# Performance work log

Measured on AMD Instinct MI355X. Metric: run time of the kernel, lower is better.

## Reference

```python
import jax, jax.numpy as jnp
import numpy as np

B, T, D = 2, 2048, 1024
NUM_HEAD = 8
HEAD_DIM = D // NUM_HEAD
CLIP = 2  # _RELATIVE_POS_CLIP


def setup_inputs() -> dict:
    key = jax.random.key(0)
    ks = jax.random.split(key, 12)
    s = 0.02
    return {
        "query": jax.random.normal(ks[0], (B, T, D), jnp.float32),
        "keys": jax.random.normal(ks[1], (B, T, D), jnp.float32),
        "values": jax.random.normal(ks[2], (B, T, D), jnp.float32),
        "Wq": jax.random.normal(ks[3], (D, D), jnp.float32) * s,
        "bq": jnp.zeros((D,), jnp.float32),
        "Wk": jax.random.normal(ks[4], (D, D), jnp.float32) * s,
        "bk": jnp.zeros((D,), jnp.float32),
        "Wv": jax.random.normal(ks[5], (D, D), jnp.float32) * s,
        "bv": jnp.zeros((D,), jnp.float32),
        "Wo": jax.random.normal(ks[6], (D, D), jnp.float32) * s,
        "bo": jnp.zeros((D,), jnp.float32),
        "relpos_table": jax.random.normal(ks[7], (2 * CLIP + 1, D), jnp.float32) * s,
    }


def reference(query, keys, values, Wq, bq, Wk, bk, Wv, bv, Wo, bo, relpos_table):
    Bq, T2, _ = query.shape
    T1 = keys.shape[1]
    # QKV projections (torch Linear: y = x @ W.T + b)
    tq = query @ Wq.T + bq                      # (B, T2, D)
    tk = keys @ Wk.T + bk                       # (B, T1, D)
    tv = values @ Wv.T + bv                     # (B, T1, D)

    # relative-position logits: relpos_embed[i,j] = table[clip(j-i)+CLIP]
    # faithful math via (B,T2,5) dots + gather instead of (T2,T1,D) broadcast
    relpos = jnp.clip(jnp.arange(T1)[None, :] - jnp.arange(T2)[:, None],
                      -CLIP, CLIP) + CLIP        # (T2, T1) int
    proj = tq @ relpos_table.T                   # (B, T2, 2*CLIP+1)
    relpos_logits = proj[:, jnp.arange(T2)[:, None], relpos]  # (B, T2, T1)

    # split heads
    q = tq.reshape(Bq, T2, NUM_HEAD, HEAD_DIM).transpose(0, 2, 1, 3)
    k = tk.reshape(Bq, T1, NUM_HEAD, HEAD_DIM).transpose(0, 2, 1, 3)
    v = tv.reshape(Bq, T1, NUM_HEAD, HEAD_DIM).transpose(0, 2, 1, 3)

    logits = jnp.einsum("bhqd,bhkd->bhqk", q, k)
    logits = (logits + relpos_logits[:, None]) / jnp.sqrt(
        jnp.asarray(HEAD_DIM, logits.dtype))    # scaling after bias, as in nmtlab
    weights = jax.nn.softmax(logits, axis=-1)   # (B, H, T2, T1)
    ctx = jnp.einsum("bhqk,bhkd->bhqd", weights, v)
    ctx = ctx.transpose(0, 2, 1, 3).reshape(Bq, T2, NUM_HEAD * HEAD_DIM)
    out = ctx @ Wo.T + bo                        # (B, T2, D)
    return out, weights
```

## Files before the change

kernel.cpp:

```cpp
#include <hip/hip_runtime.h>
#include <hip/hip_bf16.h>
#include <cmath>

#define Bsz 2
#define Tsz 2048
#define Dsz 1024
#define Hn  8
#define DH  128
#define SCALE 0.08838834764831845f

typedef __attribute__((ext_vector_type(8))) short short8;
typedef __attribute__((ext_vector_type(4))) short short4v;
typedef __attribute__((ext_vector_type(4))) float f32x4;
typedef __hip_bfloat16 bf16;

#define LDK 136

__device__ __forceinline__ float bf2f(unsigned short u) {
    return __uint_as_float(((unsigned)u) << 16);
}
__device__ __forceinline__ unsigned short f2bf(float f) {
    bf16 h = __float2bfloat16(f);
    return *(unsigned short*)&h;
}
__device__ __forceinline__ short8 pack8(float4 a, float4 b) {
    short8 o;
    o[0] = (short)f2bf(a.x); o[1] = (short)f2bf(a.y);
    o[2] = (short)f2bf(a.z); o[3] = (short)f2bf(a.w);
    o[4] = (short)f2bf(b.x); o[5] = (short)f2bf(b.y);
    o[6] = (short)f2bf(b.z); o[7] = (short)f2bf(b.w);
    return o;
}

__device__ __forceinline__ void gload16(const bf16* g, bf16* l) {
    __builtin_amdgcn_global_load_lds(
        (const __attribute__((address_space(1))) void*)g,
        (__attribute__((address_space(3))) void*)l, 16, 0, 0);
}

struct CvtJob { const float* s; bf16* d; int n; };
struct CvtArgs { CvtJob j[4]; };

__global__ __launch_bounds__(256) void cvt_k(CvtArgs a) {
    CvtJob job = a.j[blockIdx.y];
    int idx = (blockIdx.x * 256 + threadIdx.x) * 8;
    const int stride = gridDim.x * 256 * 8;
    for (; idx < job.n; idx += stride) {
        float4 f0 = *(const float4*)(job.s + idx);
        float4 f1 = *(const float4*)(job.s + idx + 4);
        *(short8*)(job.d + idx) = pack8(f0, f1);
    }
}

__device__ __forceinline__ void mfma_step32(const bf16* As, const bf16* Bs,
                                            f32x4 acc[4][4],
                                            int wr, int wc, int fr, int g)
{
    short8 af[4], bfv[4];
#pragma unroll
    for (int m = 0; m < 4; ++m)
        af[m] = *(const short8*)(As + (wr * 64 + m * 16 + fr) * 32 + g * 8);
#pragma unroll
    for (int n = 0; n < 4; ++n)
        bfv[n] = *(const short8*)(Bs + (wc * 64 + n * 16 + fr) * 32 + g * 8);
#pragma unroll
    for (int m = 0; m < 4; ++m)
#pragma unroll
        for (int n = 0; n < 4; ++n)
            acc[m][n] = __builtin_amdgcn_mfma_f32_16x16x32_bf16(
                af[m], bfv[n], acc[m][n], 0, 0, 0);
}

struct GemmJob { const float* A; const bf16* B; const float* bias; void* C; int mode; };
struct GemmArgs { GemmJob j[3]; };

__global__ __launch_bounds__(256, 3) void gemm_qkv_k(GemmArgs args)
{
    __shared__ __align__(16) bf16 As[128 * 32];
    __shared__ __align__(16) bf16 Bs[128 * 32];
    const int bid = blockIdx.x;
    const int wid = (bid & 7) * 96 + (bid >> 3);
    const GemmJob job = args.j[wid >> 8];
    const int t = wid & 255;
    const int row0 = (t >> 3) * 128;
    const int col0 = (t & 7) * 128;
    const int tid = threadIdx.x;
    const int lane = tid & 63;
    const int w = tid >> 6, wr = w >> 1, wc = w & 1;
    const int fr = lane & 15, g = lane >> 4;

    const int srow = lane >> 2, scol = (lane & 3) * 8;
    const float* Ag0 = job.A + (size_t)(row0 + w * 32 + srow) * Dsz + scol;
    const float* Ag1 = Ag0 + 16 * Dsz;
    const bf16*  Bg  = job.B + (size_t)(col0 + w * 32 + srow) * Dsz + scol;
    const int lofs = __builtin_amdgcn_readfirstlane(w * 1024);
    bf16* Bsw = Bs + lofs;
    bf16* Aw0 = As + lofs + lane * 8;
    bf16* Aw1 = Aw0 + 16 * 32;

    f32x4 acc[4][4];
    const f32x4 vz = {0.f, 0.f, 0.f, 0.f};
#pragma unroll
    for (int m = 0; m < 4; ++m)
#pragma unroll
        for (int n = 0; n < 4; ++n) acc[m][n] = vz;

    float4 fa0 = *(const float4*)(Ag0);
    float4 fa1 = *(const float4*)(Ag0 + 4);
    float4 fa2 = *(const float4*)(Ag1);
    float4 fa3 = *(const float4*)(Ag1 + 4);

#pragma unroll 1
    for (int k0 = 0; k0 < Dsz; k0 += 32) {
        __syncthreads();
        *(short8*)Aw0 = pack8(fa0, fa1);
        *(short8*)Aw1 = pack8(fa2, fa3);
        gload16(Bg + k0, Bsw);
        gload16(Bg + 16 * Dsz + k0, Bsw + 16 * 32);
        __syncthreads();
        if (k0 + 32 < Dsz) {
            fa0 = *(const float4*)(Ag0 + k0 + 32);
            fa1 = *(const float4*)(Ag0 + k0 + 36);
            fa2 = *(const float4*)(Ag1 + k0 + 32);
            fa3 = *(const float4*)(Ag1 + k0 + 36);
        }
        mfma_step32(As, Bs, acc, wr, wc, fr, g);
    }

    if (job.mode == 2) {
        bf16* vtp = (bf16*)job.C;
#pragma unroll
        for (int m = 0; m < 4; ++m) {
            const int gi0 = row0 + wr * 64 + m * 16 + g * 4;
            const int bidx = gi0 >> 11, jj = gi0 & 2047;
#pragma unroll
            for (int n = 0; n < 4; ++n) {
                const int gj = col0 + wc * 64 + n * 16 + fr;
                const float bv = job.bias[gj];
                short4v pk;
#pragma unroll
                for (int r = 0; r < 4; ++r)
                    pk[r] = (short)f2bf(acc[m][n][r] + bv);
                const size_t zrow = ((size_t)bidx * 8 + (gj >> 7)) * 128 + (gj & 127);
                *(short4v*)(vtp + zrow * Tsz + jj) = pk;
            }
        }
    } else {
#pragma unroll
        for (int m = 0; m < 4; ++m) {
#pragma unroll
            for (int r = 0; r < 4; ++r) {
                const int gi = row0 + wr * 64 + m * 16 + g * 4 + r;
#pragma unroll
                for (int n = 0; n < 4; ++n) {
                    const int gj = col0 + wc * 64 + n * 16 + fr;
                    float x = acc[m][n][r] + job.bias[gj];
                    ((bf16*)job.C)[(size_t)gi * Dsz + gj] = __float2bfloat16(x);
                }
            }
        }
    }
}

__global__ __launch_bounds__(256) void relproj_k(
    const bf16* __restrict__ tq, const float* __restrict__ table,
    float* __restrict__ proj)
{
    const int row  = blockIdx.x * 4 + (threadIdx.x >> 6);
    const int lane = threadIdx.x & 63;
    const bf16* qrow = tq + (size_t)row * Dsz;
    float acc[5] = {0.f, 0.f, 0.f, 0.f, 0.f};
#pragma unroll
    for (int t = 0; t < 4; ++t) {
        const int d = t * 256 + lane * 4;
        short4v q4 = *(const short4v*)(qrow + d);
        float qv[4];
#pragma unroll
        for (int q = 0; q < 4; ++q) qv[q] = bf2f((unsigned short)q4[q]);
#pragma unroll
        for (int c = 0; c < 5; ++c) {
            float4 t4 = *(const float4*)(table + c * Dsz + d);
            acc[c] = fmaf(qv[0], t4.x, acc[c]);
            acc[c] = fmaf(qv[1], t4.y, acc[c]);
            acc[c] = fmaf(qv[2], t4.z, acc[c]);
            acc[c] = fmaf(qv[3], t4.w, acc[c]);
        }
    }
#pragma unroll
    for (int c = 0; c < 5; ++c)
        for (int off = 32; off > 0; off >>= 1)
            acc[c] += __shfl_xor(acc[c], off);
    if (lane == 0) {
#pragma unroll
        for (int c = 0; c < 5; ++c)
            proj[(size_t)row * 8 + c] = acc[c];
    }
}

__global__ __launch_bounds__(512) void flash_pv_k(
    const bf16* __restrict__ tq, const bf16* __restrict__ tk,
    const bf16* __restrict__ vt, const float* __restrict__ proj,
    float* __restrict__ invs_g, bf16* __restrict__ ctx)
{
    __shared__ __align__(16) bf16 Ks[128 * LDK];
    __shared__ __align__(16) bf16 Vs[128 * LDK];
    __shared__ __align__(16) bf16 Ps[128 * 128];
    __shared__ float proj_s[5 * 132];

    const int tid = threadIdx.x;
    const int bid = blockIdx.x;
    const int wid = (bid & 7) * 32 + (bid >> 3);
    const int qt = wid & 15, z = wid >> 4;
    const int b = z >> 3, h = z & 7;
    const int i0 = qt * 128;
    const int lane = tid & 63, w = tid >> 6;
    const int fr = lane & 15, g = lane >> 4;
    const int il = w * 16 + fr;
    const int srow = tid >> 2, scb = (tid & 3) * 32;

    if (tid < 128) {
        const float* pr = proj + (size_t)(b * Tsz + i0 + tid) * 8;
#pragma unroll
        for (int c = 0; c < 5; ++c) proj_s[c * 132 + tid] = pr[c];
    }

    const bf16* qrow = tq + (size_t)(b * Tsz + i0 + il) * Dsz + h * DH + g * 8;
    short8 qf[4];
#pragma unroll
    for (int ks = 0; ks < 4; ++ks)
        qf[ks] = *(const short8*)(qrow + ks * 32);

    f32x4 accp[8];
    const f32x4 vz = {0.f, 0.f, 0.f, 0.f};
#pragma unroll
    for (int n = 0; n < 8; ++n) accp[n] = vz;
    float rs = 0.f;

    const bf16* kg = tk + (size_t)(b * Tsz + srow) * Dsz + h * DH + scb;
    const bf16* vg = vt + ((size_t)z * DH + srow) * Tsz + scb;
    short8 kv[4], vv[4];
#pragma unroll
    for (int q = 0; q < 4; ++q) kv[q] = *(const short8*)(kg + q * 8);
#pragma unroll
    for (int q = 0; q < 4; ++q) vv[q] = *(const short8*)(vg + q * 8);

#pragma unroll 1
    for (int kt = 0; kt < Tsz / 128; ++kt) {
        __syncthreads();
#pragma unroll
        for (int q = 0; q < 4; ++q) *(short8*)(Ks + srow * LDK + scb + q * 8) = kv[q];
#pragma unroll
        for (int q = 0; q < 4; ++q) *(short8*)(Vs + srow * LDK + scb + q * 8) = vv[q];
        __syncthreads();

        if (kt + 1 < Tsz / 128) {
            const bf16* kn = kg + (size_t)(kt + 1) * 128 * Dsz;
            const bf16* vn = vg + (kt + 1) * 128;
#pragma unroll
            for (int q = 0; q < 4; ++q) kv[q] = *(const short8*)(kn + q * 8);
#pragma unroll
            for (int q = 0; q < 4; ++q) vv[q] = *(const short8*)(vn + q * 8);
        }

        f32x4 as_[8];
#pragma unroll
        for (int m = 0; m < 8; ++m) as_[m] = vz;
        __builtin_amdgcn_s_setprio(1);
#pragma unroll
        for (int ks = 0; ks < 4; ++ks) {
            short8 kf[8];
#pragma unroll
            for (int mj = 0; mj < 8; ++mj)
                kf[mj] = *(const short8*)(Ks + (mj * 16 + fr) * LDK + ks * 32 + g * 8);
#pragma unroll
            for (int mj = 0; mj < 8; ++mj)
                as_[mj] = __builtin_amdgcn_mfma_f32_16x16x32_bf16(
                    kf[mj], qf[ks], as_[mj], 0, 0, 0);
        }
        __builtin_amdgcn_s_setprio(0);

        const int dt = kt - qt;
        const int pbase = il * 256;
        const int swz = (il & 7) << 4;
        if (dt <= -2 || dt >= 2) {
            const float bias = proj_s[((dt >= 2) ? 4 : 0) * 132 + il];
#pragma unroll
            for (int mj = 0; mj < 8; ++mj) {
                const int jl0 = mj * 16 + g * 4;
                short4v pk;
#pragma unroll
                for (int r = 0; r < 4; ++r) {
                    float p = __expf((as_[mj][r] + bias) * SCALE);
                    rs += p;
                    pk[r] = (short)f2bf(p);
                }
                *(short4v*)((char*)Ps + ((pbase + jl0 * 2) ^ swz)) = pk;
            }
        } else {
#pragma unroll
            for (int mj = 0; mj < 8; ++mj) {
                const int jl0 = mj * 16 + g * 4;
                short4v pk;
#pragma unroll
                for (int r = 0; r < 4; ++r) {
                    int dd = (jl0 + r + dt * 128) - il;
                    dd = dd < -2 ? -2 : (dd > 2 ? 2 : dd);
                    const float bias = proj_s[(dd + 2) * 132 + il];
                    float p = __expf((as_[mj][r] + bias) * SCALE);
                    rs += p;
                    pk[r] = (short)f2bf(p);
                }
                *(short4v*)((char*)Ps + ((pbase + jl0 * 2) ^ swz)) = pk;
            }
        }

        __builtin_amdgcn_s_setprio(1);
#pragma unroll
        for (int ks = 0; ks < 4; ++ks) {
            short8 pf = *(const short8*)((char*)Ps +
                            ((pbase + (ks * 32 + g * 8) * 2) ^ swz));
            short8 vf[8];
#pragma unroll
            for (int n2 = 0; n2 < 8; ++n2)
                vf[n2] = *(const short8*)(Vs + (n2 * 16 + fr) * LDK + ks * 32 + g * 8);
#pragma unroll
            for (int n2 = 0; n2 < 8; ++n2)
                accp[n2] = __builtin_amdgcn_mfma_f32_16x16x32_bf16(
                    pf, vf[n2], accp[n2], 0, 0, 0);
        }
        __builtin_amdgcn_s_setprio(0);
    }

    rs += __shfl_xor(rs, 16);
    rs += __shfl_xor(rs, 32);
    const float iv = 1.0f / rs;
    if (g == 0)
        invs_g[(size_t)z * Tsz + i0 + il] = iv;

    float ivr[4];
#pragma unroll
    for (int r = 0; r < 4; ++r) ivr[r] = __shfl(iv, g * 4 + r);

    bf16* cp = ctx + (size_t)(b * Tsz + i0 + w * 16) * Dsz + h * DH;
#pragma unroll
    for (int r = 0; r < 4; ++r) {
        const int irow = g * 4 + r;
#pragma unroll
        for (int n2 = 0; n2 < 8; ++n2)
            cp[(size_t)irow * Dsz + n2 * 16 + fr] = __float2bfloat16(accp[n2][r] * ivr[r]);
    }
}

__global__ __launch_bounds__(512) void wo_k(
    const bf16* __restrict__ tq, const bf16* __restrict__ tk,
    const float* __restrict__ proj, const float* __restrict__ invs_g,
    float* __restrict__ Wt,
    const bf16* __restrict__ ctx, const bf16* __restrict__ Wob,
    const float* __restrict__ bo, float* __restrict__ out)
{
    __shared__ __align__(16) bf16 As[256 * 32];
    __shared__ __align__(16) bf16 Bs[256 * 32];
    __shared__ float proj_s[5 * 264];
    __shared__ float inv_s[256];

    const int tid = threadIdx.x;
    const int lane = tid & 63, w = tid >> 6;
    const int fr = lane & 15, g = lane >> 4;
    const int wj = w & 3, wi = w >> 2;
    const int srow = lane >> 2, scol = (lane & 3) * 8;
    const int lofs = __builtin_amdgcn_readfirstlane(w * 1024);
    bf16* Asw = As + lofs;
    bf16* Bsw = Bs + lofs;
    const f32x4 vz = {0.f, 0.f, 0.f, 0.f};
    const int bid = blockIdx.x;

    if (bid >= 64) {
        const int b0 = bid - 64;
        const int wid = (b0 & 7) * 128 + (b0 >> 3);
        const int z = wid >> 6;
        const int t = wid & 63;
        const int row0 = (t >> 3) * 256;
        const int col0 = (t & 7) * 256;
        const int b = z >> 3, h = z & 7;

        if (tid < 256) {
            const float* pr = proj + (size_t)(b * Tsz + row0 + tid) * 8;
#pragma unroll
            for (int c = 0; c < 5; ++c) proj_s[c * 264 + tid] = pr[c];
        } else {
            inv_s[tid - 256] = invs_g[(size_t)z * Tsz + row0 + (tid - 256)];
        }

        const bf16* Ag = tk + (size_t)(b * Tsz + col0 + w * 32 + srow) * Dsz + h * DH + scol;
        const bf16* Bg = tq + (size_t)(b * Tsz + row0 + w * 32 + srow) * Dsz + h * DH + scol;

        f32x4 acc[4][8];
#pragma unroll
        for (int m = 0; m < 4; ++m)
#pragma unroll
            for (int n = 0; n < 8; ++n) acc[m][n] = vz;

#pragma unroll 1
        for (int k0 = 0; k0 < DH; k0 += 32) {
            __syncthreads();
            gload16(Ag + k0, Asw);
            gload16(Ag + 16 * Dsz + k0, Asw + 16 * 32);
            gload16(Bg + k0, Bsw);
            gload16(Bg + 16 * Dsz + k0, Bsw + 16 * 32);
            __syncthreads();
            short8 af[4], bfv[8];
#pragma unroll
            for (int jf = 0; jf < 4; ++jf)
                af[jf] = *(const short8*)(As + (wj * 64 + jf * 16 + fr) * 32 + g * 8);
#pragma unroll
            for (int ii = 0; ii < 8; ++ii)
                bfv[ii] = *(const short8*)(Bs + (wi * 128 + ii * 16 + fr) * 32 + g * 8);
#pragma unroll
            for (int jf = 0; jf < 4; ++jf)
#pragma unroll
                for (int ii = 0; ii < 8; ++ii)
                    acc[jf][ii] = __builtin_amdgcn_mfma_f32_16x16x32_bf16(
                        af[jf], bfv[ii], acc[jf][ii], 0, 0, 0);
        }

        float* C = Wt + (size_t)z * Tsz * Tsz;
        const int dmin = col0 - (row0 + 255);
        const int dmax = (col0 + 255) - row0;
        if (dmin >= 2 || dmax <= -2) {
            const int c = (dmin >= 2) ? 4 : 0;
#pragma unroll
            for (int ii = 0; ii < 8; ++ii) {
                const int il = wi * 128 + ii * 16 + fr;
                const int gi = row0 + il;
                const float iv = inv_s[il];
                const float bias = proj_s[c * 264 + il];
#pragma unroll
                for (int jf = 0; jf < 4; ++jf) {
                    const int jb = col0 + wj * 64 + jf * 16 + g * 4;
                    float4 o;
                    float* op = (float*)&o;
#pragma unroll
                    for (int r = 0; r < 4; ++r)
                        op[r] = __expf((acc[jf][ii][r] + bias) * SCALE) * iv;
                    *(float4*)(C + (size_t)gi * Tsz + jb) = o;
                }
            }
        } else {
#pragma unroll
            for (int ii = 0; ii < 8; ++ii) {
                const int il = wi * 128 + ii * 16 + fr;
                const int gi = row0 + il;
                const float iv = inv_s[il];
#pragma unroll
                for (int jf = 0; jf < 4; ++jf) {
                    const int jb = col0 + wj * 64 + jf * 16 + g * 4;
                    float4 o;
                    float* op = (float*)&o;
#pragma unroll
                    for (int r = 0; r < 4; ++r) {
                        int rel = (jb + r) - gi;
                        rel = rel < -2 ? -2 : (rel > 2 ? 2 : rel);
                        const float bias = proj_s[(rel + 2) * 264 + il];
                        op[r] = __expf((acc[jf][ii][r] + bias) * SCALE) * iv;
                    }
                    *(float4*)(C + (size_t)gi * Tsz + jb) = o;
                }
            }
        }
    } else {
        const int row0 = (bid >> 2) * 256;
        const int col0 = (bid & 3) * 256;
        const bf16* Ag = ctx + (size_t)(row0 + w * 32 + srow) * Dsz + scol;
        const bf16* Bg = Wob + (size_t)(col0 + w * 32 + srow) * Dsz + scol;

        f32x4 acc2[8][4];
#pragma unroll
        for (int m = 0; m < 8; ++m)
#pragma unroll
            for (int n = 0; n < 4; ++n) acc2[m][n] = vz;

#pragma unroll 1
        for (int k0 = 0; k0 < Dsz; k0 += 32) {
            __syncthreads();
            gload16(Ag + k0, Asw);
            gload16(Ag + 16 * Dsz + k0, Asw + 16 * 32);
            gload16(Bg + k0, Bsw);
            gload16(Bg + 16 * Dsz + k0, Bsw + 16 * 32);
            __syncthreads();
            short8 af[8], bfv[4];
#pragma unroll
            for (int ii = 0; ii < 8; ++ii)
                af[ii] = *(const short8*)(As + (wi * 128 + ii * 16 + fr) * 32 + g * 8);
#pragma unroll
            for (int jc = 0; jc < 4; ++jc)
                bfv[jc] = *(const short8*)(Bs + (wj * 64 + jc * 16 + fr) * 32 + g * 8);
#pragma unroll
            for (int ii = 0; ii < 8; ++ii)
#pragma unroll
                for (int jc = 0; jc < 4; ++jc)
                    acc2[ii][jc] = __builtin_amdgcn_mfma_f32_16x16x32_bf16(
                        af[ii], bfv[jc], acc2[ii][jc], 0, 0, 0);
        }

#pragma unroll
        for (int ii = 0; ii < 8; ++ii) {
#pragma unroll
            for (int r = 0; r < 4; ++r) {
                const int gi = row0 + wi * 128 + ii * 16 + g * 4 + r;
#pragma unroll
                for (int jc = 0; jc < 4; ++jc) {
                    const int gj = col0 + wj * 64 + jc * 16 + fr;
                    out[(size_t)gi * Dsz + gj] = acc2[ii][jc][r] + bo[gj];
                }
            }
        }
    }
}

extern "C" void kernel_launch(void* const* d_in, const int* in_sizes, int n_in,
                              void* d_out, int out_size, void* d_ws, size_t ws_size,
                              hipStream_t stream)
{
    const float* query  = (const float*)d_in[0];
    const float* keys   = (const float*)d_in[1];
    const float* values = (const float*)d_in[2];
    const float* Wq = (const float*)d_in[3];
    const float* bq = (const float*)d_in[4];
    const float* Wk = (const float*)d_in[5];
    const float* bk = (const float*)d_in[6];
    const float* Wv = (const float*)d_in[7];
    const float* bv = (const float*)d_in[8];
    const float* Wo = (const float*)d_in[9];
    const float* bo = (const float*)d_in[10];
    const float* table = (const float*)d_in[11];

    float* out     = (float*)d_out;
    float* weights = out + (size_t)Bsz * Tsz * Dsz;

    char* wp = (char*)d_ws;
    bf16* tq  = (bf16*)(wp);
    bf16* tk  = (bf16*)(wp + 8  * 1024 * 1024);
    bf16* vt  = (bf16*)(wp + 16 * 1024 * 1024);
    bf16* ctx = (bf16*)(wp + 24 * 1024 * 1024);
    bf16* Wqb = (bf16*)(wp + 32 * 1024 * 1024);
    bf16* Wkb = (bf16*)(wp + 34 * 1024 * 1024);
    bf16* Wvb = (bf16*)(wp + 36 * 1024 * 1024);
    bf16* Wob = (bf16*)(wp + 38 * 1024 * 1024);
    float* proj   = (float*)(wp + 40 * 1024 * 1024);
    float* invs_g = (float*)(wp + 41 * 1024 * 1024);

    const dim3 blk(256);

    CvtArgs ca;
    ca.j[0] = { Wq, Wqb, Dsz * Dsz };
    ca.j[1] = { Wk, Wkb, Dsz * Dsz };
    ca.j[2] = { Wv, Wvb, Dsz * Dsz };
    ca.j[3] = { Wo, Wob, Dsz * Dsz };
    cvt_k<<<dim3(128, 4), blk, 0, stream>>>(ca);

    GemmArgs ga;
    ga.j[0] = { query,  Wqb, bq, tq, 1 };
    ga.j[1] = { keys,   Wkb, bk, tk, 1 };
    ga.j[2] = { values, Wvb, bv, vt, 2 };
    gemm_qkv_k<<<dim3(768), blk, 0, stream>>>(ga);

    relproj_k<<<dim3(Bsz * Tsz / 4), blk, 0, stream>>>(tq, table, proj);

    flash_pv_k<<<dim3(256), dim3(512), 0, stream>>>(
        tq, tk, vt, proj, invs_g, ctx);

    wo_k<<<dim3(64 + 1024), dim3(512), 0, stream>>>(
        tq, tk, proj, invs_g, weights, ctx, Wob, bo, out);
}
```

Baseline: 205.3 us.

## Give each flash warp two query row tiles and use nontemporal weight stores

The flash attention kernel drops from 512 to 256 threads per block, and each wave now handles 32 query rows (two 16-row MFMA tiles) instead of 16. This reuses every K and V fragment read from LDS across two MFMAs, cutting LDS traffic per FLOP, but it doubles the accumulator registers per thread and halves the number of waves per block. Separately, the softmax-weights writes in wo_k switch to nontemporal stores so the large 128MB output does not pollute the cache.

```diff
diff --git a/kernel.cpp b/kernel.cpp
--- a/kernel.cpp
+++ b/kernel.cpp
@@ -197,7 +197,7 @@
     }
 }
 
-__global__ __launch_bounds__(512) void flash_pv_k(
+__global__ __launch_bounds__(256) void flash_pv_k(
     const bf16* __restrict__ tq, const bf16* __restrict__ tk,
     const bf16* __restrict__ vt, const float* __restrict__ proj,
     float* __restrict__ invs_g, bf16* __restrict__ ctx)
@@ -215,8 +215,8 @@
     const int i0 = qt * 128;
     const int lane = tid & 63, w = tid >> 6;
     const int fr = lane & 15, g = lane >> 4;
-    const int il = w * 16 + fr;
-    const int srow = tid >> 2, scb = (tid & 3) * 32;
+    const int il0 = w * 32 + fr;
+    const int srow = tid >> 1, scb = (tid & 1) * 64;
 
     if (tid < 128) {
         const float* pr = proj + (size_t)(b * Tsz + i0 + tid) * 8;
@@ -224,47 +224,54 @@
         for (int c = 0; c < 5; ++c) proj_s[c * 132 + tid] = pr[c];
     }
 
-    const bf16* qrow = tq + (size_t)(b * Tsz + i0 + il) * Dsz + h * DH + g * 8;
-    short8 qf[4];
-#pragma unroll
-    for (int ks = 0; ks < 4; ++ks)
-        qf[ks] = *(const short8*)(qrow + ks * 32);
-
-    f32x4 accp[8];
+    short8 qf[2][4];
+#pragma unroll
+    for (int ni = 0; ni < 2; ++ni) {
+        const bf16* qrow = tq + (size_t)(b * Tsz + i0 + il0 + ni * 16) * Dsz + h * DH + g * 8;
+#pragma unroll
+        for (int ks = 0; ks < 4; ++ks)
+            qf[ni][ks] = *(const short8*)(qrow + ks * 32);
+    }
+
+    f32x4 accp[2][8];
     const f32x4 vz = {0.f, 0.f, 0.f, 0.f};
 #pragma unroll
-    for (int n = 0; n < 8; ++n) accp[n] = vz;
-    float rs = 0.f;
+    for (int m = 0; m < 2; ++m)
+#pragma unroll
+        for (int n = 0; n < 8; ++n) accp[m][n] = vz;
+    float rs[2] = {0.f, 0.f};
 
     const bf16* kg = tk + (size_t)(b * Tsz + srow) * Dsz + h * DH + scb;
     const bf16* vg = vt + ((size_t)z * DH + srow) * Tsz + scb;
-    short8 kv[4], vv[4];
-#pragma unroll
-    for (int q = 0; q < 4; ++q) kv[q] = *(const short8*)(kg + q * 8);
-#pragma unroll
-    for (int q = 0; q < 4; ++q) vv[q] = *(const short8*)(vg + q * 8);
+    short8 kv[8], vv[8];
+#pragma unroll
+    for (int q = 0; q < 8; ++q) kv[q] = *(const short8*)(kg + q * 8);
+#pragma unroll
+    for (int q = 0; q < 8; ++q) vv[q] = *(const short8*)(vg + q * 8);
 
 #pragma unroll 1
     for (int kt = 0; kt < Tsz / 128; ++kt) {
         __syncthreads();
 #pragma unroll
-        for (int q = 0; q < 4; ++q) *(short8*)(Ks + srow * LDK + scb + q * 8) = kv[q];
-#pragma unroll
-        for (int q = 0; q < 4; ++q) *(short8*)(Vs + srow * LDK + scb + q * 8) = vv[q];
+        for (int q = 0; q < 8; ++q) *(short8*)(Ks + srow * LDK + scb + q * 8) = kv[q];
+#pragma unroll
+        for (int q = 0; q < 8; ++q) *(short8*)(Vs + srow * LDK + scb + q * 8) = vv[q];
         __syncthreads();
 
         if (kt + 1 < Tsz / 128) {
             const bf16* kn = kg + (size_t)(kt + 1) * 128 * Dsz;
             const bf16* vn = vg + (kt + 1) * 128;
 #pragma unroll
-            for (int q = 0; q < 4; ++q) kv[q] = *(const short8*)(kn + q * 8);
-#pragma unroll
-            for (int q = 0; q < 4; ++q) vv[q] = *(const short8*)(vn + q * 8);
-        }
-
-        f32x4 as_[8];
-#pragma unroll
-        for (int m = 0; m < 8; ++m) as_[m] = vz;
+            for (int q = 0; q < 8; ++q) kv[q] = *(const short8*)(kn + q * 8);
+#pragma unroll
+            for (int q = 0; q < 8; ++q) vv[q] = *(const short8*)(vn + q * 8);
+        }
+
+        f32x4 as_[2][8];
+#pragma unroll
+        for (int ni = 0; ni < 2; ++ni)
+#pragma unroll
+            for (int m = 0; m < 8; ++m) as_[ni][m] = vz;
         __builtin_amdgcn_s_setprio(1);
 #pragma unroll
         for (int ks = 0; ks < 4; ++ks) {
@@ -273,81 +280,107 @@
             for (int mj = 0; mj < 8; ++mj)
                 kf[mj] = *(const short8*)(Ks + (mj * 16 + fr) * LDK + ks * 32 + g * 8);
 #pragma unroll
-            for (int mj = 0; mj < 8; ++mj)
-                as_[mj] = __builtin_amdgcn_mfma_f32_16x16x32_bf16(
-                    kf[mj], qf[ks], as_[mj], 0, 0, 0);
+            for (int mj = 0; mj < 8; ++mj) {
+                as_[0][mj] = __builtin_amdgcn_mfma_f32_16x16x32_bf16(
+                    kf[mj], qf[0][ks], as_[0][mj], 0, 0, 0);
+                as_[1][mj] = __builtin_amdgcn_mfma_f32_16x16x32_bf16(
+                    kf[mj], qf[1][ks], as_[1][mj], 0, 0, 0);
+            }
         }
         __builtin_amdgcn_s_setprio(0);
 
         const int dt = kt - qt;
-        const int pbase = il * 256;
-        const int swz = (il & 7) << 4;
-        if (dt <= -2 || dt >= 2) {
-            const float bias = proj_s[((dt >= 2) ? 4 : 0) * 132 + il];
-#pragma unroll
-            for (int mj = 0; mj < 8; ++mj) {
-                const int jl0 = mj * 16 + g * 4;
-                short4v pk;
-#pragma unroll
-                for (int r = 0; r < 4; ++r) {
-                    float p = __expf((as_[mj][r] + bias) * SCALE);
-                    rs += p;
-                    pk[r] = (short)f2bf(p);
+#pragma unroll
+        for (int ni = 0; ni < 2; ++ni) {
+            const int il = il0 + ni * 16;
+            const int pbase = il * 256;
+            const int swz = (il & 7) << 4;
+            if (dt <= -2 || dt >= 2) {
+                const float bias = proj_s[((dt >= 2) ? 4 : 0) * 132 + il];
+#pragma unroll
+                for (int mj = 0; mj < 8; ++mj) {
+                    const int jl0 = mj * 16 + g * 4;
+                    short4v pk;
+#pragma unroll
+                    for (int r = 0; r < 4; ++r) {
+                        float p = __expf((as_[ni][mj][r] + bias) * SCALE);
+                        rs[ni] += p;
+                        pk[r] = (short)f2bf(p);
+                    }
+                    *(short4v*)((char*)Ps + ((pbase + jl0 * 2) ^ swz)) = pk;
                 }
-                *(short4v*)((char*)Ps + ((pbase + jl0 * 2) ^ swz)) = pk;
-            }
-        } else {
-#pragma unroll
-            for (int mj = 0; mj < 8; ++mj) {
-                const int jl0 = mj * 16 + g * 4;
-                short4v pk;
-#pragma unroll
-                for (int r = 0; r < 4; ++r) {
-                    int dd = (jl0 + r + dt * 128) - il;
-                    dd = dd < -2 ? -2 : (dd > 2 ? 2 : dd);
-                    const float bias = proj_s[(dd + 2) * 132 + il];
-                    float p = __expf((as_[mj][r] + bias) * SCALE);
-                    rs += p;
-                    pk[r] = (short)f2bf(p);
+            } else {
+#pragma unroll
+                for (int mj = 0; mj < 8; ++mj) {
+                    const int jl0 = mj * 16 + g * 4;
+                    short4v pk;
+#pragma unroll
+                    for (int r = 0; r < 4; ++r) {
+                        int dd = (jl0 + r + dt * 128) - il;
+                        dd = dd < -2 ? -2 : (dd > 2 ? 2 : dd);
+                        const float bias = proj_s[(dd + 2) * 132 + il];
+                        float p = __expf((as_[ni][mj][r] + bias) * SCALE);
+                        rs[ni] += p;
+                        pk[r] = (short)f2bf(p);
+                    }
+                    *(short4v*)((char*)Ps + ((pbase + jl0 * 2) ^ swz)) = pk;
                 }
-                *(short4v*)((char*)Ps + ((pbase + jl0 * 2) ^ swz)) = pk;
             }
         }
 
         __builtin_amdgcn_s_setprio(1);
 #pragma unroll
         for (int ks = 0; ks < 4; ++ks) {
-            short8 pf = *(const short8*)((char*)Ps +
-                            ((pbase + (ks * 32 + g * 8) * 2) ^ swz));
-            short8 vf[8];
+            short8 pf[2], vf[8];
+#pragma unroll
+            for (int m = 0; m < 2; ++m) {
+                const int il = il0 + m * 16;
+                pf[m] = *(const short8*)((char*)Ps +
+                            ((il * 256 + (ks * 32 + g * 8) * 2) ^ ((il & 7) << 4)));
+            }
 #pragma unroll
             for (int n2 = 0; n2 < 8; ++n2)
                 vf[n2] = *(const short8*)(Vs + (n2 * 16 + fr) * LDK + ks * 32 + g * 8);
 #pragma unroll
+            for (int m = 0; m < 2; ++m)
+#pragma unroll
+                for (int n2 = 0; n2 < 8; ++n2)
+                    accp[m][n2] = __builtin_amdgcn_mfma_f32_16x16x32_bf16(
+                        pf[m], vf[n2], accp[m][n2], 0, 0, 0);
+        }
+        __builtin_amdgcn_s_setprio(0);
+    }
+
+#pragma unroll
+    for (int ni = 0; ni < 2; ++ni) {
+        rs[ni] += __shfl_xor(rs[ni], 16);
+        rs[ni] += __shfl_xor(rs[ni], 32);
+    }
+    const float iv0 = 1.0f / rs[0];
+    const float iv1 = 1.0f / rs[1];
+    if (g == 0) {
+        invs_g[(size_t)z * Tsz + i0 + il0]      = iv0;
+        invs_g[(size_t)z * Tsz + i0 + il0 + 16] = iv1;
+    }
+
+    float ivr[2][4];
+#pragma unroll
+    for (int r = 0; r < 4; ++r) {
+        ivr[0][r] = __shfl(iv0, g * 4 + r);
+        ivr[1][r] = __shfl(iv1, g * 4 + r);
+    }
+
+    bf16* cp = ctx + (size_t)(b * Tsz + i0 + w * 32) * Dsz + h * DH;
+#pragma unroll
+    for (int ni = 0; ni < 2; ++ni) {
+#pragma unroll
+        for (int r = 0; r < 4; ++r) {
+            const int irow = ni * 16 + g * 4 + r;
+#pragma unroll
             for (int n2 = 0; n2 < 8; ++n2)
-                accp[n2] = __builtin_amdgcn_mfma_f32_16x16x32_bf16(
-                    pf, vf[n2], accp[n2], 0, 0, 0);
-        }
-        __builtin_amdgcn_s_setprio(0);
-    }
-
-    rs += __shfl_xor(rs, 16);
-    rs += __shfl_xor(rs, 32);
-    const float iv = 1.0f / rs;
-    if (g == 0)
-        invs_g[(size_t)z * Tsz + i0 + il] = iv;
-
-    float ivr[4];
-#pragma unroll
-    for (int r = 0; r < 4; ++r) ivr[r] = __shfl(iv, g * 4 + r);
-
-    bf16* cp = ctx + (size_t)(b * Tsz + i0 + w * 16) * Dsz + h * DH;
-#pragma unroll
-    for (int r = 0; r < 4; ++r) {
-        const int irow = g * 4 + r;
-#pragma unroll
-        for (int n2 = 0; n2 < 8; ++n2)
-            cp[(size_t)irow * Dsz + n2 * 16 + fr] = __float2bfloat16(accp[n2][r] * ivr[r]);
+                cp[(size_t)irow * Dsz + n2 * 16 + fr] =
+                    __float2bfloat16(accp[ni][n2][r] * ivr[ni][r]);
+        }
     }
 }
 
@@ -437,12 +470,11 @@
 #pragma unroll
                 for (int jf = 0; jf < 4; ++jf) {
                     const int jb = col0 + wj * 64 + jf * 16 + g * 4;
-                    float4 o;
-                    float* op = (float*)&o;
+                    f32x4 o;
 #pragma unroll
                     for (int r = 0; r < 4; ++r)
-                        op[r] = __expf((acc[jf][ii][r] + bias) * SCALE) * iv;
-                    *(float4*)(C + (size_t)gi * Tsz + jb) = o;
+                        o[r] = __expf((acc[jf][ii][r] + bias) * SCALE) * iv;
+                    __builtin_nontemporal_store(o, (f32x4*)(C + (size_t)gi * Tsz + jb));
                 }
             }
         } else {
@@ -454,16 +486,15 @@
 #pragma unroll
                 for (int jf = 0; jf < 4; ++jf) {
                     const int jb = col0 + wj * 64 + jf * 16 + g * 4;
-                    float4 o;
-                    float* op = (float*)&o;
+                    f32x4 o;
 #pragma unroll
                     for (int r = 0; r < 4; ++r) {
                         int rel = (jb + r) - gi;
                         rel = rel < -2 ? -2 : (rel > 2 ? 2 : rel);
                         const float bias = proj_s[(rel + 2) * 264 + il];
-                        op[r] = __expf((acc[jf][ii][r] + bias) * SCALE) * iv;
+                        o[r] = __expf((acc[jf][ii][r] + bias) * SCALE) * iv;
                     }
-                    *(float4*)(C + (size_t)gi * Tsz + jb) = o;
+                    __builtin_nontemporal_store(o, (f32x4*)(C + (size_t)gi * Tsz + jb));
                 }
             }
         }
@@ -566,7 +597,7 @@
 
     relproj_k<<<dim3(Bsz * Tsz / 4), blk, 0, stream>>>(tq, table, proj);
 
-    flash_pv_k<<<dim3(256), dim3(512), 0, stream>>>(
+    flash_pv_k<<<dim3(256), dim3(256), 0, stream>>>(
         tq, tk, vt, proj, invs_g, ctx);
 
     wo_k<<<dim3(64 + 1024), dim3(512), 0, stream>>>(
```

Measured after the change: 211.1 us. +2.9%, slower.
